# Kernel optimization log

Measured on AMD Instinct MI355X. Metric: run time of the kernel, lower is better.

## Reference

```python
import jax, jax.numpy as jnp
import numpy as np

LN_EPS = 1e-5


def _forward(x, conv_w, conv_b, ln_w, ln_b, in_proj_w, in_proj_b, out_proj_w, out_proj_b):
    # x: (1, duration, dimensions)
    B, Dur, Dim = x.shape
    xt = jnp.transpose(x, (0, 2, 1))  # (1, Dim, Dur) -> Conv1d NCH layout
    branches = []
    for b in range(Dur):  # structural loop over the 32 conv branches (kernel size k=b+1)
        k = b + 1
        L = Dur - b  # output length duration - k + 1
        w = conv_w[b, :, :, :k]  # (Dim_out, Dim_in, k); padded taps beyond k unused
        y = jax.lax.conv_general_dilated(
            xt, w, window_strides=(1,), padding='VALID',
            dimension_numbers=('NCH', 'OIH', 'NCH'))  # (1, Dim, L)
        y = y + conv_b[b][None, :, None]
        y = jax.nn.gelu(y, approximate=False)  # torch nn.GELU default is exact erf form
        # LayerNorm(normalized_shape=[1, Dim, L]) with batch==1 normalizes the whole tensor
        mu = jnp.mean(y)
        var = jnp.var(y)  # biased, matching torch LayerNorm
        y = (y - mu) * jax.lax.rsqrt(var + LN_EPS)
        y = y * ln_w[b, :, :L][None] + ln_b[b, :, :L][None]
        branches.append(y)  # dropout is identity at inference (p=0.0)
    xc = jnp.concatenate(branches, axis=2)  # (1, Dim, T), T = Dur*(Dur+1)//2
    T = xc.shape[2]

    # nn.MultiheadAttention(embed_dim=T, num_heads=T), batch_first=False: input (L=1, N=Dim, E=T).
    # With seq_len==1, softmax over the single key is exactly 1, so attention output is
    # out_proj(v_proj(value)). value_i = x[:, i, :] broadcast over N, so every batch row of
    # output_i equals out_proj(v_proj(xc[0, i])). Summing over i (the feature loop):
    Wv = in_proj_w[2 * T:]          # (T, T) value slice of in_proj
    bv = in_proj_b[2 * T:]          # (T,)
    V = xc[0] @ Wv.T + bv           # (Dim, T): row i is v-proj of feature i
    S = V.sum(axis=0) @ out_proj_w.T + Dim * out_proj_b  # (T,)  sum over the Dim-term loop
    xa = jnp.broadcast_to(S[None, None, :], (1, Dim, T))  # identical rows, as in torch

    # x.unfold(2, Dur, 4*Dur).mean(-1)
    step = 4 * Dur
    n_w = (T - Dur) // step + 1
    idx = jnp.arange(n_w)[:, None] * step + jnp.arange(Dur)[None, :]  # (n_w, Dur)
    pooled = xa[:, :, idx].mean(-1)  # (1, Dim, n_w)
    return jnp.transpose(pooled, (0, 2, 1))  # (1, n_w, Dim)


def setup_inputs() -> dict:
    key = jax.random.key(0)
    ks = jax.random.split(key, 6)
    Dur, Dim = 32, 256
    T = Dur * (Dur + 1) // 2  # 528
    x = jax.random.normal(ks[0], (1, Dur, Dim), jnp.float32)
    conv_w = jax.random.normal(ks[1], (Dur, Dim, Dim, Dur), jnp.float32) * 0.02  # padded kernel bank
    conv_b = jax.random.normal(ks[2], (Dur, Dim), jnp.float32) * 0.02
    ln_w = jnp.ones((Dur, Dim, Dur), jnp.float32)   # branch b uses [:, :, :Dur-b]
    ln_b = jnp.zeros((Dur, Dim, Dur), jnp.float32)
    in_proj_w = jax.random.normal(ks[3], (3 * T, T), jnp.float32) * 0.02
    in_proj_b = jnp.zeros((3 * T,), jnp.float32)
    out_proj_w = jax.random.normal(ks[4], (T, T), jnp.float32) * 0.02
    out_proj_b = jnp.zeros((T,), jnp.float32)
    return {"x": x, "conv_w": conv_w, "conv_b": conv_b, "ln_w": ln_w, "ln_b": ln_b,
            "in_proj_w": in_proj_w, "in_proj_b": in_proj_b,
            "out_proj_w": out_proj_w, "out_proj_b": out_proj_b}


def reference(x, conv_w, conv_b, ln_w, ln_b, in_proj_w, in_proj_b, out_proj_w, out_proj_b):
    return _forward(x, conv_w, conv_b, ln_w, ln_b, in_proj_w, in_proj_b, out_proj_w, out_proj_b)
```

## Files before the change

kernel.cpp:

```cpp
#include <hip/hip_runtime.h>
#include <math.h>

#define DUR 32
#define DIM 256
#define TT  528

#define WS_BSUM 0
#define WS_BSQ  32
#define WS_CY   64
#define WS_CW   592
#define WS_CB   1120
#define WS_S    1648
#define WS_S2   2176
#define WS_ZERO_FLOATS 1648

__device__ __forceinline__ float gelu_exact(float v) {
    return 0.5f * v * (1.0f + erff(v * 0.70710678118654752f));
}

template<int K4>
__device__ __forceinline__ void conv_body(
    const int bb, const int o0, const int tid,
    const float* __restrict__ x, const float* __restrict__ W,
    const float* __restrict__ convb, const float* __restrict__ lnw,
    const float* __restrict__ lnb, float* __restrict__ ws,
    char* __restrict__ smem, float (* __restrict__ red)[4][32],
    float (* __restrict__ epi)[4][32], float (* __restrict__ sred)[2])
{
    constexpr bool DB  = (K4 < 8);
    constexpr int BUFB = 256 * 16 * K4;
    const int k = bb + 1;
    const int L = 32 - bb;
    const int wave = tid >> 6;
    const int lane = tid & 63;

    float xv[35];
#pragma unroll
    for (int tau = 0; tau < 32; ++tau) xv[tau] = x[tau * DIM + tid];
    xv[32] = 0.f; xv[33] = 0.f; xv[34] = 0.f;

    const float* Wb = W + (size_t)bb * (DIM * DIM * DUR) + (size_t)o0 * (DIM * DUR);

    float4 wreg[K4];
    auto issue = [&](int oo) {
#pragma unroll
        for (int r = 0; r < K4; ++r) {
            const int e = r * 256 + tid;
            wreg[r] = *(const float4*)(Wb + (size_t)oo * (DIM * DUR)
                                        + (e / K4) * 32 + (e % K4) * 4);
        }
    };
    auto stage = [&](int p) {
#pragma unroll
        for (int r = 0; r < K4; ++r) {
            const int e = r * 256 + tid;
            const int n = e / K4, m = e % K4;
            *(float4*)(smem + p * BUFB + (n * K4 + (m + n) % K4) * 16) = wreg[r];
        }
    };

    float cy = 0.f, cw = 0.f, cbv = 0.f, s1 = 0.f, s2 = 0.f;

    auto epilogue = [&](int j) {
        const int o = o0 + j;
        float g = 0.f;
        if (lane < L) {
            const float y = red[j & 1][0][lane] + red[j & 1][1][lane]
                          + red[j & 1][2][lane] + red[j & 1][3][lane]
                          + convb[bb * DIM + o];
            g = gelu_exact(y);
            const float lw = lnw[((size_t)(bb * DIM + o)) * DUR + lane];
            const float lb = lnb[((size_t)(bb * DIM + o)) * DUR + lane];
            cy += g * lw; cw += lw; cbv += lb;
        }
        s1 += g; s2 += g * g;
    };

    issue(0);
#pragma unroll
    for (int oo = 0; oo < 8; ++oo) {
        const int p = DB ? (oo & 1) : 0;
        if (!DB && oo > 0) __syncthreads();
        stage(p);
        __syncthreads();
        if (oo < 7) issue(oo + 1);

        if (oo > 0 && wave == ((oo - 1) & 3)) epilogue(oo - 1);

        float acc[32];
#pragma unroll
        for (int t = 0; t < 32; ++t) acc[t] = 0.f;

        const char* myrow = smem + p * BUFB + tid * (16 * K4);
#pragma unroll
        for (int m = 0; m < K4; ++m) {
            float4 w4 = *(const float4*)(myrow + ((m + tid) % K4) * 16);
            if (4 * m + 0 >= k) w4.x = 0.f;
            if (4 * m + 1 >= k) w4.y = 0.f;
            if (4 * m + 2 >= k) w4.z = 0.f;
            if (4 * m + 3 >= k) w4.w = 0.f;
#pragma unroll
            for (int t = 0; t < 32; ++t) {
                if (t < L) {
                    acc[t] = fmaf(xv[t + 4*m + 0], w4.x, acc[t]);
                    acc[t] = fmaf(xv[t + 4*m + 1], w4.y, acc[t]);
                    acc[t] = fmaf(xv[t + 4*m + 2], w4.z, acc[t]);
                    acc[t] = fmaf(xv[t + 4*m + 3], w4.w, acc[t]);
                }
            }
        }

#pragma unroll
        for (int t = 0; t < 32; ++t) {
            if (t < L) {
                float v = acc[t];
                v += __shfl_down(v, 32, 64);
                v += __shfl_down(v, 16, 64);
                v += __shfl_down(v, 8, 64);
                v += __shfl_down(v, 4, 64);
                v += __shfl_down(v, 2, 64);
                v += __shfl_down(v, 1, 64);
                if (lane == 0) red[oo & 1][wave][t] = v;
            }
        }
    }
    __syncthreads();
    if (wave == 3) epilogue(7);

    if (lane < 32) {
        epi[0][wave][lane] = cy;
        epi[1][wave][lane] = cw;
        epi[2][wave][lane] = cbv;
    }
    {
        float a = s1, b2 = s2;
        a += __shfl_down(a, 32, 64);  b2 += __shfl_down(b2, 32, 64);
        a += __shfl_down(a, 16, 64);  b2 += __shfl_down(b2, 16, 64);
        a += __shfl_down(a, 8, 64);   b2 += __shfl_down(b2, 8, 64);
        a += __shfl_down(a, 4, 64);   b2 += __shfl_down(b2, 4, 64);
        a += __shfl_down(a, 2, 64);   b2 += __shfl_down(b2, 2, 64);
        a += __shfl_down(a, 1, 64);   b2 += __shfl_down(b2, 1, 64);
        if (lane == 0) { sred[wave][0] = a; sred[wave][1] = b2; }
    }
    __syncthreads();
    if (wave == 0 && lane < L) {
        const int tg = bb * 32 - (bb * (bb - 1)) / 2 + lane;
        atomicAdd(ws + WS_CY + tg, epi[0][0][lane] + epi[0][1][lane] + epi[0][2][lane] + epi[0][3][lane]);
        atomicAdd(ws + WS_CW + tg, epi[1][0][lane] + epi[1][1][lane] + epi[1][2][lane] + epi[1][3][lane]);
        atomicAdd(ws + WS_CB + tg, epi[2][0][lane] + epi[2][1][lane] + epi[2][2][lane] + epi[2][3][lane]);
    }
    if (tid == 0) {
        atomicAdd(ws + WS_BSUM + bb, sred[0][0] + sred[1][0] + sred[2][0] + sred[3][0]);
        atomicAdd(ws + WS_BSQ  + bb, sred[0][1] + sred[1][1] + sred[2][1] + sred[3][1]);
    }
}

__global__ __launch_bounds__(256) void conv_kernel(
    const float* __restrict__ x, const float* __restrict__ W,
    const float* __restrict__ convb, const float* __restrict__ lnw,
    const float* __restrict__ lnb, float* ws)
{
    __shared__ char  smem[57344];
    __shared__ float red[2][4][32];
    __shared__ float epi[3][4][32];
    __shared__ float sred[4][2];

    const int bid = blockIdx.x;
    const int bb  = 31 - (bid & 31);
    const int o0  = (bid >> 5) * 8;
    const int tid = threadIdx.x;

    switch (bb >> 2) {
        case 0: conv_body<1>(bb, o0, tid, x, W, convb, lnw, lnb, ws, smem, red, epi, sred); break;
        case 1: conv_body<2>(bb, o0, tid, x, W, convb, lnw, lnb, ws, smem, red, epi, sred); break;
        case 2: conv_body<3>(bb, o0, tid, x, W, convb, lnw, lnb, ws, smem, red, epi, sred); break;
        case 3: conv_body<4>(bb, o0, tid, x, W, convb, lnw, lnb, ws, smem, red, epi, sred); break;
        case 4: conv_body<5>(bb, o0, tid, x, W, convb, lnw, lnb, ws, smem, red, epi, sred); break;
        case 5: conv_body<6>(bb, o0, tid, x, W, convb, lnw, lnb, ws, smem, red, epi, sred); break;
        case 6: conv_body<7>(bb, o0, tid, x, W, convb, lnw, lnb, ws, smem, red, epi, sred); break;
        default: conv_body<8>(bb, o0, tid, x, W, convb, lnw, lnb, ws, smem, red, epi, sred); break;
    }
}

__global__ __launch_bounds__(256) void proj1_kernel(
    float* ws, const float* __restrict__ in_proj_w,
    const float* __restrict__ in_proj_b)
{
    __shared__ float cc[TT];
    __shared__ float mu_s[32], r_s[32];
    __shared__ int map[TT];
    const int n = threadIdx.x;
    if (n < 32) {
        const int Lb = 32 - n;
        const float cnt = 256.f * (float)Lb;
        const float mu = ws[WS_BSUM + n] / cnt;
        const float var = ws[WS_BSQ + n] / cnt - mu * mu;
        mu_s[n] = mu;
        r_s[n] = rsqrtf(var + 1e-5f);
        const int off = n * 32 - (n * (n - 1)) / 2;
        for (int t = 0; t < Lb; ++t) map[off + t] = n;
    }
    __syncthreads();
    for (int t = n; t < TT; t += 256) {
        const int b = map[t];
        cc[t] = (ws[WS_CY + t] - mu_s[b] * ws[WS_CW + t]) * r_s[b] + ws[WS_CB + t];
    }
    __syncthreads();
    const int wave = n >> 6, lane = n & 63;
    const int row = blockIdx.x * 4 + wave;
    const float* Wr = in_proj_w + (size_t)(2 * TT + row) * TT;
    float a = 0.f;
    for (int t = lane; t < TT; t += 64) a = fmaf(Wr[t], cc[t], a);
    a += __shfl_down(a, 32, 64);
    a += __shfl_down(a, 16, 64);
    a += __shfl_down(a, 8, 64);
    a += __shfl_down(a, 4, 64);
    a += __shfl_down(a, 2, 64);
    a += __shfl_down(a, 1, 64);
    if (lane == 0) ws[WS_S + row] = a + 256.f * in_proj_b[2 * TT + row];
}

__global__ __launch_bounds__(256) void proj2a_kernel(
    float* ws, const float* __restrict__ out_proj_w,
    const float* __restrict__ out_proj_b)
{
    const int i = blockIdx.x;
    const int u = (i >> 5) * 128 + (i & 31);
    const int n = threadIdx.x;
    const int wave = n >> 6, lane = n & 63;
    const float* Or = out_proj_w + (size_t)u * TT;
    float a = 0.f;
    for (int t = n; t < TT; t += 256) a = fmaf(Or[t], ws[WS_S + t], a);
    a += __shfl_down(a, 32, 64);
    a += __shfl_down(a, 16, 64);
    a += __shfl_down(a, 8, 64);
    a += __shfl_down(a, 4, 64);
    a += __shfl_down(a, 2, 64);
    a += __shfl_down(a, 1, 64);
    __shared__ float r4[4];
    if (lane == 0) r4[wave] = a;
    __syncthreads();
    if (n == 0) ws[WS_S2 + i] = r4[0] + r4[1] + r4[2] + r4[3] + 256.f * out_proj_b[u];
}

__global__ __launch_bounds__(256) void proj2b_kernel(
    const float* __restrict__ ws, float* __restrict__ out)
{
    const int n = threadIdx.x;
    __shared__ float mv;
    if (n < 64) {
        float v = (n < 32) ? ws[WS_S2 + blockIdx.x * 32 + n] : 0.f;
        v += __shfl_down(v, 16, 64);
        v += __shfl_down(v, 8, 64);
        v += __shfl_down(v, 4, 64);
        v += __shfl_down(v, 2, 64);
        v += __shfl_down(v, 1, 64);
        if (n == 0) mv = v * (1.0f / 32.0f);
    }
    __syncthreads();
    out[blockIdx.x * 256 + n] = mv;
}

extern "C" void kernel_launch(void* const* d_in, const int* in_sizes, int n_in,
                              void* d_out, int out_size, void* d_ws, size_t ws_size,
                              hipStream_t stream)
{
    const float* x   = (const float*)d_in[0];
    const float* W   = (const float*)d_in[1];
    const float* cb  = (const float*)d_in[2];
    const float* lnw = (const float*)d_in[3];
    const float* lnb = (const float*)d_in[4];
    const float* ipw = (const float*)d_in[5];
    const float* ipb = (const float*)d_in[6];
    const float* opw = (const float*)d_in[7];
    const float* opb = (const float*)d_in[8];
    float* ws  = (float*)d_ws;
    float* out = (float*)d_out;

    hipMemsetAsync(ws, 0, WS_ZERO_FLOATS * sizeof(float), stream);
    conv_kernel<<<1024, 256, 0, stream>>>(x, W, cb, lnw, lnb, ws);
    proj1_kernel<<<132, 256, 0, stream>>>(ws, ipw, ipb);
    proj2a_kernel<<<128, 256, 0, stream>>>(ws, opw, opb);
    proj2b_kernel<<<4, 256, 0, stream>>>(ws, out);
}
```

Baseline: 445.9 us.

## Deepen weight prefetch, split branch stats into separate kernel, merge projection kernels

Conv kernel now prefetches two output channels ahead for small kernel widths, sizes accumulators by the maximum output length per template, and writes raw conv outputs to workspace. GELU, LayerNorm statistics and the per-position weighted sums move to a new per-branch kernel, which removes the atomics and the memset. The two out-projection kernels are merged into one with 4 blocks. The gain is less register pressure and fewer atomics; the cost is an extra launch, an extra workspace round trip, and lower parallelism in the 4-block projection.

```diff
diff --git a/kernel.cpp b/kernel.cpp
--- a/kernel.cpp
+++ b/kernel.cpp
@@ -5,14 +5,9 @@
 #define DIM 256
 #define TT  528
 
-#define WS_BSUM 0
-#define WS_BSQ  32
-#define WS_CY   64
-#define WS_CW   592
-#define WS_CB   1120
-#define WS_S    1648
-#define WS_S2   2176
-#define WS_ZERO_FLOATS 1648
+#define WS_C 0
+#define WS_S 528
+#define WS_Y 2048
 
 __device__ __forceinline__ float gelu_exact(float v) {
     return 0.5f * v * (1.0f + erff(v * 0.70710678118654752f));
@@ -22,17 +17,14 @@
 __device__ __forceinline__ void conv_body(
     const int bb, const int o0, const int tid,
     const float* __restrict__ x, const float* __restrict__ W,
-    const float* __restrict__ convb, const float* __restrict__ lnw,
-    const float* __restrict__ lnb, float* __restrict__ ws,
-    char* __restrict__ smem, float (* __restrict__ red)[4][32],
-    float (* __restrict__ epi)[4][32], float (* __restrict__ sred)[2])
-{
-    constexpr bool DB  = (K4 < 8);
-    constexpr int BUFB = 256 * 16 * K4;
+    float* __restrict__ ws, char* __restrict__ smem, float (* __restrict__ red)[4][32])
+{
+    constexpr int Lmax  = 36 - 4 * K4;
+    constexpr int DEPTH = (K4 <= 4) ? 2 : 1;
+    constexpr int BUFB  = 256 * 16 * K4;
     const int k = bb + 1;
     const int L = 32 - bb;
-    const int wave = tid >> 6;
-    const int lane = tid & 63;
+    const int wave = tid >> 6, lane = tid & 63;
 
     float xv[35];
 #pragma unroll
@@ -41,56 +33,29 @@
 
     const float* Wb = W + (size_t)bb * (DIM * DIM * DUR) + (size_t)o0 * (DIM * DUR);
 
-    float4 wreg[K4];
-    auto issue = [&](int oo) {
+    float4 wregA[K4];
+    float4 wregB[DEPTH == 2 ? K4 : 1];
+
+    auto issue = [&](int oo, float4* dst) {
 #pragma unroll
         for (int r = 0; r < K4; ++r) {
             const int e = r * 256 + tid;
-            wreg[r] = *(const float4*)(Wb + (size_t)oo * (DIM * DUR)
-                                        + (e / K4) * 32 + (e % K4) * 4);
-        }
-    };
-    auto stage = [&](int p) {
+            const int n = e / K4, m = e - n * K4;
+            dst[r] = *(const float4*)(Wb + (size_t)oo * (DIM * DUR) + n * 32 + m * 4);
+        }
+    };
+    auto stage = [&](int p, const float4* src) {
 #pragma unroll
         for (int r = 0; r < K4; ++r) {
             const int e = r * 256 + tid;
-            const int n = e / K4, m = e % K4;
-            *(float4*)(smem + p * BUFB + (n * K4 + (m + n) % K4) * 16) = wreg[r];
-        }
-    };
-
-    float cy = 0.f, cw = 0.f, cbv = 0.f, s1 = 0.f, s2 = 0.f;
-
-    auto epilogue = [&](int j) {
-        const int o = o0 + j;
-        float g = 0.f;
-        if (lane < L) {
-            const float y = red[j & 1][0][lane] + red[j & 1][1][lane]
-                          + red[j & 1][2][lane] + red[j & 1][3][lane]
-                          + convb[bb * DIM + o];
-            g = gelu_exact(y);
-            const float lw = lnw[((size_t)(bb * DIM + o)) * DUR + lane];
-            const float lb = lnb[((size_t)(bb * DIM + o)) * DUR + lane];
-            cy += g * lw; cw += lw; cbv += lb;
-        }
-        s1 += g; s2 += g * g;
-    };
-
-    issue(0);
-#pragma unroll
-    for (int oo = 0; oo < 8; ++oo) {
-        const int p = DB ? (oo & 1) : 0;
-        if (!DB && oo > 0) __syncthreads();
-        stage(p);
-        __syncthreads();
-        if (oo < 7) issue(oo + 1);
-
-        if (oo > 0 && wave == ((oo - 1) & 3)) epilogue(oo - 1);
-
-        float acc[32];
-#pragma unroll
-        for (int t = 0; t < 32; ++t) acc[t] = 0.f;
-
+            const int n = e / K4, m = e - n * K4;
+            *(float4*)(smem + p * BUFB + (n * K4 + (m + n) % K4) * 16) = src[r];
+        }
+    };
+    auto compute = [&](int p) {
+        float acc[Lmax];
+#pragma unroll
+        for (int t = 0; t < Lmax; ++t) acc[t] = 0.f;
         const char* myrow = smem + p * BUFB + tid * (16 * K4);
 #pragma unroll
         for (int m = 0; m < K4; ++m) {
@@ -100,7 +65,7 @@
             if (4 * m + 2 >= k) w4.z = 0.f;
             if (4 * m + 3 >= k) w4.w = 0.f;
 #pragma unroll
-            for (int t = 0; t < 32; ++t) {
+            for (int t = 0; t < Lmax; ++t) {
                 if (t < L) {
                     acc[t] = fmaf(xv[t + 4*m + 0], w4.x, acc[t]);
                     acc[t] = fmaf(xv[t + 4*m + 1], w4.y, acc[t]);
@@ -109,9 +74,8 @@
                 }
             }
         }
-
-#pragma unroll
-        for (int t = 0; t < 32; ++t) {
+#pragma unroll
+        for (int t = 0; t < Lmax; ++t) {
             if (t < L) {
                 float v = acc[t];
                 v += __shfl_down(v, 32, 64);
@@ -120,50 +84,57 @@
                 v += __shfl_down(v, 4, 64);
                 v += __shfl_down(v, 2, 64);
                 v += __shfl_down(v, 1, 64);
-                if (lane == 0) red[oo & 1][wave][t] = v;
+                if (lane == 0) red[p][wave][t] = v;
             }
         }
+    };
+    auto epilogue = [&](int j) {
+        const int o = o0 + j;
+        if (lane < L) {
+            const int q = j & 1;
+            const float y = red[q][0][lane] + red[q][1][lane]
+                          + red[q][2][lane] + red[q][3][lane];
+            ws[WS_Y + bb * 8192 + o * 32 + lane] = y;
+        }
+    };
+
+    if constexpr (DEPTH == 2) {
+        issue(0, wregA);
+        issue(1, wregB);
+#pragma unroll
+        for (int s = 0; s < 4; ++s) {
+            const int ooA = 2 * s, ooB = 2 * s + 1;
+            stage(0, wregA);
+            __syncthreads();
+            if (ooA + 2 < 8) issue(ooA + 2, wregA);
+            if (ooA > 0 && wave == ((ooA - 1) & 3)) epilogue(ooA - 1);
+            compute(0);
+            stage(1, wregB);
+            __syncthreads();
+            if (ooB + 2 < 8) issue(ooB + 2, wregB);
+            if (wave == ((ooB - 1) & 3)) epilogue(ooB - 1);
+            compute(1);
+        }
+    } else {
+        issue(0, wregA);
+#pragma unroll
+        for (int oo = 0; oo < 8; ++oo) {
+            stage(oo & 1, wregA);
+            __syncthreads();
+            if (oo + 1 < 8) issue(oo + 1, wregA);
+            if (oo > 0 && wave == ((oo - 1) & 3)) epilogue(oo - 1);
+            compute(oo & 1);
+        }
     }
     __syncthreads();
     if (wave == 3) epilogue(7);
-
-    if (lane < 32) {
-        epi[0][wave][lane] = cy;
-        epi[1][wave][lane] = cw;
-        epi[2][wave][lane] = cbv;
-    }
-    {
-        float a = s1, b2 = s2;
-        a += __shfl_down(a, 32, 64);  b2 += __shfl_down(b2, 32, 64);
-        a += __shfl_down(a, 16, 64);  b2 += __shfl_down(b2, 16, 64);
-        a += __shfl_down(a, 8, 64);   b2 += __shfl_down(b2, 8, 64);
-        a += __shfl_down(a, 4, 64);   b2 += __shfl_down(b2, 4, 64);
-        a += __shfl_down(a, 2, 64);   b2 += __shfl_down(b2, 2, 64);
-        a += __shfl_down(a, 1, 64);   b2 += __shfl_down(b2, 1, 64);
-        if (lane == 0) { sred[wave][0] = a; sred[wave][1] = b2; }
-    }
-    __syncthreads();
-    if (wave == 0 && lane < L) {
-        const int tg = bb * 32 - (bb * (bb - 1)) / 2 + lane;
-        atomicAdd(ws + WS_CY + tg, epi[0][0][lane] + epi[0][1][lane] + epi[0][2][lane] + epi[0][3][lane]);
-        atomicAdd(ws + WS_CW + tg, epi[1][0][lane] + epi[1][1][lane] + epi[1][2][lane] + epi[1][3][lane]);
-        atomicAdd(ws + WS_CB + tg, epi[2][0][lane] + epi[2][1][lane] + epi[2][2][lane] + epi[2][3][lane]);
-    }
-    if (tid == 0) {
-        atomicAdd(ws + WS_BSUM + bb, sred[0][0] + sred[1][0] + sred[2][0] + sred[3][0]);
-        atomicAdd(ws + WS_BSQ  + bb, sred[0][1] + sred[1][1] + sred[2][1] + sred[3][1]);
-    }
-}
-
-__global__ __launch_bounds__(256) void conv_kernel(
-    const float* __restrict__ x, const float* __restrict__ W,
-    const float* __restrict__ convb, const float* __restrict__ lnw,
-    const float* __restrict__ lnb, float* ws)
-{
-    __shared__ char  smem[57344];
+}
+
+__global__ __launch_bounds__(256, 4) void conv_kernel(
+    const float* __restrict__ x, const float* __restrict__ W, float* __restrict__ ws)
+{
+    __shared__ char  smem[65536];
     __shared__ float red[2][4][32];
-    __shared__ float epi[3][4][32];
-    __shared__ float sred[4][2];
 
     const int bid = blockIdx.x;
     const int bb  = 31 - (bid & 31);
@@ -171,40 +142,73 @@
     const int tid = threadIdx.x;
 
     switch (bb >> 2) {
-        case 0: conv_body<1>(bb, o0, tid, x, W, convb, lnw, lnb, ws, smem, red, epi, sred); break;
-        case 1: conv_body<2>(bb, o0, tid, x, W, convb, lnw, lnb, ws, smem, red, epi, sred); break;
-        case 2: conv_body<3>(bb, o0, tid, x, W, convb, lnw, lnb, ws, smem, red, epi, sred); break;
-        case 3: conv_body<4>(bb, o0, tid, x, W, convb, lnw, lnb, ws, smem, red, epi, sred); break;
-        case 4: conv_body<5>(bb, o0, tid, x, W, convb, lnw, lnb, ws, smem, red, epi, sred); break;
-        case 5: conv_body<6>(bb, o0, tid, x, W, convb, lnw, lnb, ws, smem, red, epi, sred); break;
-        case 6: conv_body<7>(bb, o0, tid, x, W, convb, lnw, lnb, ws, smem, red, epi, sred); break;
-        default: conv_body<8>(bb, o0, tid, x, W, convb, lnw, lnb, ws, smem, red, epi, sred); break;
+        case 0: conv_body<1>(bb, o0, tid, x, W, ws, smem, red); break;
+        case 1: conv_body<2>(bb, o0, tid, x, W, ws, smem, red); break;
+        case 2: conv_body<3>(bb, o0, tid, x, W, ws, smem, red); break;
+        case 3: conv_body<4>(bb, o0, tid, x, W, ws, smem, red); break;
+        case 4: conv_body<5>(bb, o0, tid, x, W, ws, smem, red); break;
+        case 5: conv_body<6>(bb, o0, tid, x, W, ws, smem, red); break;
+        case 6: conv_body<7>(bb, o0, tid, x, W, ws, smem, red); break;
+        default: conv_body<8>(bb, o0, tid, x, W, ws, smem, red); break;
+    }
+}
+
+__global__ __launch_bounds__(256) void branch_kernel(
+    const float* __restrict__ convb, const float* __restrict__ lnw,
+    const float* __restrict__ lnb, float* __restrict__ ws)
+{
+    const int b = blockIdx.x;
+    const int L = 32 - b;
+    const int tid = threadIdx.x;
+    const int wave = tid >> 6, lane = tid & 63;
+
+    float a1 = 0.f, a2 = 0.f, a3 = 0.f, s1 = 0.f, s2 = 0.f;
+    for (int oi = 0; oi < 64; ++oi) {
+        const int o = wave * 64 + oi;
+        float g = 0.f;
+        if (lane < L) {
+            const float y = ws[WS_Y + b * 8192 + o * 32 + lane] + convb[b * DIM + o];
+            g = gelu_exact(y);
+            const float lw = lnw[(size_t)(b * DIM + o) * DUR + lane];
+            const float lb = lnb[(size_t)(b * DIM + o) * DUR + lane];
+            a1 += g * lw; a2 += lw; a3 += lb;
+        }
+        s1 += g; s2 += g * g;
+    }
+    __shared__ float ra[4][32], rb2[4][32], rc[4][32], rs[4][2];
+    {
+        float u = s1, v = s2;
+        u += __shfl_xor(u, 32, 64); v += __shfl_xor(v, 32, 64);
+        u += __shfl_xor(u, 16, 64); v += __shfl_xor(v, 16, 64);
+        u += __shfl_xor(u, 8, 64);  v += __shfl_xor(v, 8, 64);
+        u += __shfl_xor(u, 4, 64);  v += __shfl_xor(v, 4, 64);
+        u += __shfl_xor(u, 2, 64);  v += __shfl_xor(v, 2, 64);
+        u += __shfl_xor(u, 1, 64);  v += __shfl_xor(v, 1, 64);
+        if (lane == 0) { rs[wave][0] = u; rs[wave][1] = v; }
+    }
+    if (lane < 32) { ra[wave][lane] = a1; rb2[wave][lane] = a2; rc[wave][lane] = a3; }
+    __syncthreads();
+    if (wave == 0 && lane < L) {
+        const float A1 = ra[0][lane] + ra[1][lane] + ra[2][lane] + ra[3][lane];
+        const float A2 = rb2[0][lane] + rb2[1][lane] + rb2[2][lane] + rb2[3][lane];
+        const float A3 = rc[0][lane] + rc[1][lane] + rc[2][lane] + rc[3][lane];
+        const float S1 = rs[0][0] + rs[1][0] + rs[2][0] + rs[3][0];
+        const float S2 = rs[0][1] + rs[1][1] + rs[2][1] + rs[3][1];
+        const float cnt = 256.f * (float)L;
+        const float mu = S1 / cnt;
+        const float r  = rsqrtf(S2 / cnt - mu * mu + 1e-5f);
+        const int boff = b * 32 - (b * (b - 1)) / 2;
+        ws[WS_C + boff + lane] = r * (A1 - mu * A2) + A3;
     }
 }
 
 __global__ __launch_bounds__(256) void proj1_kernel(
-    float* ws, const float* __restrict__ in_proj_w,
+    float* __restrict__ ws, const float* __restrict__ in_proj_w,
     const float* __restrict__ in_proj_b)
 {
     __shared__ float cc[TT];
-    __shared__ float mu_s[32], r_s[32];
-    __shared__ int map[TT];
     const int n = threadIdx.x;
-    if (n < 32) {
-        const int Lb = 32 - n;
-        const float cnt = 256.f * (float)Lb;
-        const float mu = ws[WS_BSUM + n] / cnt;
-        const float var = ws[WS_BSQ + n] / cnt - mu * mu;
-        mu_s[n] = mu;
-        r_s[n] = rsqrtf(var + 1e-5f);
-        const int off = n * 32 - (n * (n - 1)) / 2;
-        for (int t = 0; t < Lb; ++t) map[off + t] = n;
-    }
-    __syncthreads();
-    for (int t = n; t < TT; t += 256) {
-        const int b = map[t];
-        cc[t] = (ws[WS_CY + t] - mu_s[b] * ws[WS_CW + t]) * r_s[b] + ws[WS_CB + t];
-    }
+    for (int t = n; t < TT; t += 256) cc[t] = ws[WS_C + t];
     __syncthreads();
     const int wave = n >> 6, lane = n & 63;
     const int row = blockIdx.x * 4 + wave;
@@ -220,42 +224,38 @@
     if (lane == 0) ws[WS_S + row] = a + 256.f * in_proj_b[2 * TT + row];
 }
 
-__global__ __launch_bounds__(256) void proj2a_kernel(
-    float* ws, const float* __restrict__ out_proj_w,
-    const float* __restrict__ out_proj_b)
-{
-    const int i = blockIdx.x;
-    const int u = (i >> 5) * 128 + (i & 31);
+__global__ __launch_bounds__(256) void proj2_kernel(
+    const float* __restrict__ ws, const float* __restrict__ out_proj_w,
+    const float* __restrict__ out_proj_b, float* __restrict__ out)
+{
+    __shared__ float sv[TT];
+    __shared__ float Sacc[32];
+    __shared__ float mv;
     const int n = threadIdx.x;
+    for (int t = n; t < TT; t += 256) sv[t] = ws[WS_S + t];
+    __syncthreads();
     const int wave = n >> 6, lane = n & 63;
-    const float* Or = out_proj_w + (size_t)u * TT;
-    float a = 0.f;
-    for (int t = n; t < TT; t += 256) a = fmaf(Or[t], ws[WS_S + t], a);
-    a += __shfl_down(a, 32, 64);
-    a += __shfl_down(a, 16, 64);
-    a += __shfl_down(a, 8, 64);
-    a += __shfl_down(a, 4, 64);
-    a += __shfl_down(a, 2, 64);
-    a += __shfl_down(a, 1, 64);
-    __shared__ float r4[4];
-    if (lane == 0) r4[wave] = a;
-    __syncthreads();
-    if (n == 0) ws[WS_S2 + i] = r4[0] + r4[1] + r4[2] + r4[3] + 256.f * out_proj_b[u];
-}
-
-__global__ __launch_bounds__(256) void proj2b_kernel(
-    const float* __restrict__ ws, float* __restrict__ out)
-{
-    const int n = threadIdx.x;
-    __shared__ float mv;
-    if (n < 64) {
-        float v = (n < 32) ? ws[WS_S2 + blockIdx.x * 32 + n] : 0.f;
-        v += __shfl_down(v, 16, 64);
-        v += __shfl_down(v, 8, 64);
-        v += __shfl_down(v, 4, 64);
-        v += __shfl_down(v, 2, 64);
-        v += __shfl_down(v, 1, 64);
-        if (n == 0) mv = v * (1.0f / 32.0f);
+#pragma unroll
+    for (int jj = 0; jj < 8; ++jj) {
+        const int j = wave * 8 + jj;
+        const int u = blockIdx.x * 128 + j;
+        const float* Or = out_proj_w + (size_t)u * TT;
+        float a = 0.f;
+        for (int t = lane; t < TT; t += 64) a = fmaf(Or[t], sv[t], a);
+        a += __shfl_down(a, 32, 64);
+        a += __shfl_down(a, 16, 64);
+        a += __shfl_down(a, 8, 64);
+        a += __shfl_down(a, 4, 64);
+        a += __shfl_down(a, 2, 64);
+        a += __shfl_down(a, 1, 64);
+        if (lane == 0) Sacc[j] = a + 256.f * out_proj_b[u];
+    }
+    __syncthreads();
+    if (n == 0) {
+        float m = 0.f;
+#pragma unroll
+        for (int j = 0; j < 32; ++j) m += Sacc[j];
+        mv = m * (1.0f / 32.0f);
     }
     __syncthreads();
     out[blockIdx.x * 256 + n] = mv;
@@ -277,9 +277,8 @@
     float* ws  = (float*)d_ws;
     float* out = (float*)d_out;
 
-    hipMemsetAsync(ws, 0, WS_ZERO_FLOATS * sizeof(float), stream);
-    conv_kernel<<<1024, 256, 0, stream>>>(x, W, cb, lnw, lnb, ws);
+    conv_kernel<<<1024, 256, 0, stream>>>(x, W, ws);
+    branch_kernel<<<32, 256, 0, stream>>>(cb, lnw, lnb, ws);
     proj1_kernel<<<132, 256, 0, stream>>>(ws, ipw, ipb);
-    proj2a_kernel<<<128, 256, 0, stream>>>(ws, opw, opb);
-    proj2b_kernel<<<4, 256, 0, stream>>>(ws, out);
-}
+    proj2_kernel<<<4, 256, 0, stream>>>(ws, opw, opb, out);
+}
```

After: 535.0 us. 20.0% more time.
